# Kernel tuning notes

Measured on AMD Instinct MI355X. Metric: run time of the kernel, lower is better.

Reference implementation:

```python
import jax, jax.numpy as jnp
import numpy as np

NEG_SLOPE = 0.01
EPS = 1e-5


def _p(key, shape, scale=0.05):
    return jax.random.normal(key, shape, dtype=jnp.float32) * scale


def setup_inputs() -> dict:
    key = jax.random.key(0)
    ks = jax.random.split(key, 20)
    B, C0, N = 256, 160, 1024
    trees = jax.random.normal(ks[0], (B, C0, N), dtype=jnp.float32)
    indexes = jax.random.randint(ks[1], (B, 3 * N), 0, N)
    nodes = jax.random.randint(ks[2], (B,), 1, N + 1)
    dims = [(160, 256), (256, 128), (128, 64)]
    inp = {"trees": trees, "indexes": indexes, "nodes": nodes}
    for i, (ci, co) in enumerate(dims, start=1):
        inp[f"Wc{i}"] = _p(ks[2 + 4 * i], (co, ci, 3))   # tree-conv weight
        inp[f"bc{i}"] = jnp.zeros((co,), jnp.float32)
        inp[f"Wm{i}"] = _p(ks[3 + 4 * i], (co, ci))       # channel-mixer (1x1) weight
        inp[f"bm{i}"] = jnp.zeros((co,), jnp.float32)
    inp["W1"] = _p(ks[16], (64, 32))
    inp["b1"] = jnp.zeros((32,), jnp.float32)
    inp["W2"] = _p(ks[17], (32, 1))
    inp["b2"] = jnp.zeros((1,), jnp.float32)
    return inp


def _lero_block(x, idx, Wc, bc, Wm, bm):
    # x: [B, C, N], idx: [B, 3N] gather indices into node axis
    B, C, N = x.shape
    g = jnp.take_along_axis(x, idx[:, None, :], axis=2)          # [B, C, 3N]
    g = g.reshape(B, C, N, 3)                                    # parent/left/right triples
    y = jnp.einsum('bcnk,ock->bon', g, Wc) + bc[None, :, None]   # BinaryTreeConv
    mu = jnp.mean(y, axis=(1, 2), keepdims=True)                 # TreeLayerNorm (per-tree)
    sd = jnp.std(y, axis=(1, 2), keepdims=True, ddof=1)
    y = (y - mu) / (sd + EPS)
    xm = jnp.einsum('bcn,oc->bon', x, Wm) + bm[None, :, None]    # ChannelMixer
    return jax.nn.leaky_relu(xm + y, NEG_SLOPE)


def reference(trees, indexes, nodes,
              Wc1, bc1, Wm1, bm1,
              Wc2, bc2, Wm2, bm2,
              Wc3, bc3, Wm3, bm3,
              W1, b1, W2, b2):
    x = _lero_block(trees, indexes, Wc1, bc1, Wm1, bm1)
    x = _lero_block(x, indexes, Wc2, bc2, Wm2, bm2)
    x = _lero_block(x, indexes, Wc3, bc3, Wm3, bm3)   # [B, 64, N]
    N = x.shape[2]
    mask = jnp.arange(N)[None, :] < nodes[:, None]     # PreciseMaxPooling: mask padding
    pooled = jnp.max(jnp.where(mask[:, None, :], x, -jnp.inf), axis=2)  # [B, 64]
    h = jax.nn.leaky_relu(pooled @ W1 + b1, NEG_SLOPE)
    return h @ W2 + b2                                  # [B, 1]
```

## Files before the change

kernel.cpp:

```cpp
#include <hip/hip_runtime.h>
#include <stdint.h>

using f16 = _Float16;
typedef __attribute__((ext_vector_type(8))) f16 f16x8;
typedef __attribute__((ext_vector_type(4))) f16 f16x4;
typedef __attribute__((ext_vector_type(4))) float f32x4;

constexpr int N = 1024;

__device__ __forceinline__ float leaky(float v) { return v >= 0.f ? v : 0.01f * v; }

__device__ __forceinline__ void dma16(const void* g, void* l) {
    __builtin_amdgcn_global_load_lds(
        (const __attribute__((address_space(1))) uint32_t*)g,
        (__attribute__((address_space(3))) uint32_t*)l, 16, 0, 0);
}

template<int CI, int CO, int SEGS, int NSTG, int UW, int RT, bool ISMIX>
__global__ __launch_bounds__(512) void gemm_kernel(
    const f16* __restrict__ X, const int* __restrict__ idx,
    const f16* __restrict__ Wf, const float* __restrict__ bias,
    f16* __restrict__ Y, float2* __restrict__ part,
    const float2* __restrict__ pin, int nparts, float Mf)
{
    constexpr int SKT = SEGS * CI / 32;
    constexpr int KS32 = (SKT + NSTG - 1) / NSTG;
    constexpr int Ug = CO / 16;
    constexpr int NGRAN = KS32 * UW * 64;
    constexpr int SBYTES = NGRAN * 16;
    constexpr int EBYTES = 8 * 16 * 68 * 4;
    constexpr int LBYTES = SBYTES > EBYTES ? SBYTES : EBYTES;
    static_assert(CI % 32 == 0 && UW % 4 == 0, "geometry");
    static_assert(RT == 1 || RT == 2, "rt");

    __shared__ alignas(16) char ldsraw[LBYTES];
    __shared__ float redu[16];

    const int tid = threadIdx.x;
    const int w = tid >> 6, l = tid & 63;
    const int n0 = blockIdx.x * (128 * RT);
    const int u0 = blockIdx.y * UW;
    const int b  = blockIdx.z;
    const int g  = blockIdx.x + gridDim.x * blockIdx.y;

    int rows[RT][SEGS];
    #pragma unroll
    for (int rt = 0; rt < RT; ++rt) {
        int n = n0 + 16 * (RT * w + rt) + (l & 15);
        if constexpr (ISMIX) {
            rows[rt][0] = n;
        } else {
            const int* ip = idx + (size_t)b * 3 * N + 3 * n;
            #pragma unroll
            for (int s = 0; s < SEGS; ++s) rows[rt][s] = ip[s];
        }
    }
    const f16* xb = X + (size_t)b * N * CI;
    const int koff = 8 * (l >> 4);

    float2 st = make_float2(0.f, 0.f);
    if constexpr (ISMIX) {
        float s1 = 0.f, s2 = 0.f;
        for (int i = 0; i < nparts; ++i) {
            float2 p = pin[(size_t)b * 16 + i];
            s1 += p.x; s2 += p.y;
        }
        float mu = s1 / Mf;
        float var = fmaxf((s2 - s1 * s1 / Mf) / (Mf - 1.f), 0.f);
        st = make_float2(mu, 1.f / (sqrtf(var) + 1e-5f));
    }

    const f16* lds = (const f16*)ldsraw;

    auto stageW = [&](int pp) {
        for (int gg = tid; gg < NGRAN; gg += 512) {
            int skk = gg / (UW * 64);
            int uu = (gg >> 6) % UW;
            int ll = gg & 63;
            int skg = pp * KS32 + skk;
            if (skg < SKT)
                dma16(Wf + (((size_t)skg * Ug + u0 + uu) * 64 + ll) * 8,
                      ldsraw + (size_t)gg * 16);
        }
    };

    f16x8 pa[RT][3];
    auto loadA = [&](int sk, int d) {
        const int seg = (sk * 32) / CI;
        const int co = sk * 32 - seg * CI + koff;
        #pragma unroll
        for (int rt = 0; rt < RT; ++rt)
            pa[rt][d] = *(const f16x8*)(xb + (size_t)rows[rt][seg] * CI + co);
    };

    if constexpr (NSTG == 1) stageW(0);

    constexpr int D = SKT < 3 ? SKT : 3;
    #pragma unroll
    for (int d = 0; d < D; ++d) loadA(d, d);

    if constexpr (NSTG == 1) __syncthreads();

    f32x4 acc[RT][UW] = {};

    #pragma unroll
    for (int pp = 0; pp < NSTG; ++pp) {
        if constexpr (NSTG > 1) { stageW(pp); __syncthreads(); }

        #pragma unroll
        for (int skl = 0; skl < KS32; ++skl) {
            const int sk = pp * KS32 + skl;
            if (sk >= SKT) break;
            f16x8 av[RT];
            #pragma unroll
            for (int rt = 0; rt < RT; ++rt) av[rt] = pa[rt][sk % 3];
            if (sk + 3 < SKT) loadA(sk + 3, sk % 3);
            #pragma unroll
            for (int uu = 0; uu < UW; ++uu) {
                f16x8 wv = *(const f16x8*)(lds + ((size_t)(skl * UW + uu) * 64 + l) * 8);
                #pragma unroll
                for (int rt = 0; rt < RT; ++rt)
                    acc[rt][uu] = __builtin_amdgcn_mfma_f32_16x16x32_f16(av[rt], wv, acc[rt][uu], 0, 0, 0);
            }
        }
        if (pp + 1 < NSTG) __syncthreads();
    }

    __syncthreads();

    float (*ep)[68] = (float(*)[68])(ldsraw + w * 4352);
    float ps1 = 0.f, ps2 = 0.f;

    #pragma unroll
    for (int rt = 0; rt < RT; ++rt) {
        #pragma unroll
        for (int E = 0; E < UW / 4; ++E) {
            asm volatile("s_waitcnt lgkmcnt(0)" ::: "memory");
            #pragma unroll
            for (int u4 = 0; u4 < 4; ++u4)
                #pragma unroll
                for (int j = 0; j < 4; ++j)
                    ep[4 * (l >> 4) + j][u4 * 16 + (l & 15)] = acc[rt][E * 4 + u4][j];
            asm volatile("s_waitcnt lgkmcnt(0)" ::: "memory");
            __builtin_amdgcn_sched_barrier(0);
            #pragma unroll
            for (int ci = 0; ci < 2; ++ci) {
                int c = l + 64 * ci;
                int r = c >> 3, oc = (c & 7) * 8;
                int ob = u0 * 16 + E * 64 + oc;
                int n = n0 + 16 * (RT * w + rt) + r;
                size_t yoff = ((size_t)b * N + n) * CO + ob;
                float v[8];
                #pragma unroll
                for (int k = 0; k < 8; ++k) v[k] = ep[r][oc + k] + bias[ob + k];
                f16x8 rv;
                if constexpr (!ISMIX) {
                    #pragma unroll
                    for (int k = 0; k < 8; ++k) {
                        ps1 += v[k]; ps2 += v[k] * v[k];
                        rv[k] = (f16)v[k];
                    }
                } else {
                    f16x8 yc = *(const f16x8*)(Y + yoff);
                    #pragma unroll
                    for (int k = 0; k < 8; ++k)
                        rv[k] = (f16)leaky(v[k] + ((float)yc[k] - st.x) * st.y);
                }
                *(f16x8*)(Y + yoff) = rv;
            }
        }
    }

    if constexpr (!ISMIX) {
        #pragma unroll
        for (int m = 32; m; m >>= 1) { ps1 += __shfl_xor(ps1, m); ps2 += __shfl_xor(ps2, m); }
        if (l == 0) { redu[w * 2] = ps1; redu[w * 2 + 1] = ps2; }
        __syncthreads();
        if (tid == 0) {
            float t1 = 0.f, t2 = 0.f;
            #pragma unroll
            for (int k = 0; k < 8; ++k) { t1 += redu[2 * k]; t2 += redu[2 * k + 1]; }
            part[(size_t)b * 16 + g] = make_float2(t1, t2);
        }
    }
}

__global__ __launch_bounds__(256) void transpose_kernel(
    const float* __restrict__ trees, f16* __restrict__ X0)
{
    __shared__ f16 tile[32][68];
    int b = blockIdx.z, c0 = blockIdx.y * 32, n0 = blockIdx.x * 64;
    int tid = threadIdx.x;
    #pragma unroll
    for (int r = 0; r < 2; ++r) {
        int s = tid + 256 * r;
        int c = s >> 4, nq = (s & 15) * 4;
        float4 v = *(const float4*)&trees[((size_t)b * 160 + c0 + c) * N + n0 + nq];
        f16x4 h; h[0] = (f16)v.x; h[1] = (f16)v.y; h[2] = (f16)v.z; h[3] = (f16)v.w;
        *(f16x4*)&tile[c][nq] = h;
    }
    __syncthreads();
    int nn = tid >> 2, gc = tid & 3;
    f16x8 pack;
    #pragma unroll
    for (int e = 0; e < 8; ++e) pack[e] = tile[gc * 8 + e][nn];
    *(f16x8*)(X0 + ((size_t)b * N + n0 + nn) * 160 + c0 + gc * 8) = pack;
}

__device__ __forceinline__ void prepW_one(
    const float* __restrict__ Wsrc, f16* __restrict__ out,
    int e, int CO, int CI, int isconv)
{
    int j = e & 7, l = (e >> 3) & 63, r = e >> 9;
    int U = CO / 16;
    int u = r % U, t = r / U;
    int kap = 32 * t + 8 * (l >> 4) + j;
    int o = 16 * u + (l & 15);
    float v = isconv ? Wsrc[((size_t)o * CI + (kap % CI)) * 3 + kap / CI]
                     : Wsrc[(size_t)o * CI + kap];
    out[e] = (f16)v;
}

__global__ __launch_bounds__(256) void prepW6_kernel(
    const float* Wc1, const float* Wm1, const float* Wc2, const float* Wm2,
    const float* Wc3, const float* Wm3,
    f16* o1, f16* m1, f16* o2, f16* m2, f16* o3, f16* m3)
{
    int bx = blockIdx.x;
    if (bx < 480)       prepW_one(Wc1, o1, (bx -    0) * 256 + threadIdx.x, 256, 160, 1);
    else if (bx < 640)  prepW_one(Wm1, m1, (bx -  480) * 256 + threadIdx.x, 256, 160, 0);
    else if (bx < 1024) prepW_one(Wc2, o2, (bx -  640) * 256 + threadIdx.x, 128, 256, 1);
    else if (bx < 1152) prepW_one(Wm2, m2, (bx - 1024) * 256 + threadIdx.x, 128, 256, 0);
    else if (bx < 1248) prepW_one(Wc3, o3, (bx - 1152) * 256 + threadIdx.x,  64, 128, 1);
    else                prepW_one(Wm3, m3, (bx - 1248) * 256 + threadIdx.x,  64, 128, 0);
}

__global__ __launch_bounds__(256) void final_kernel(
    const f16* __restrict__ x3, const int* __restrict__ nodes,
    const float* __restrict__ W1, const float* __restrict__ b1,
    const float* __restrict__ W2, const float* __restrict__ b2,
    float* __restrict__ out)
{
    int b = blockIdx.x, tid = threadIdx.x;
    int oq = (tid & 7) * 8, rr = tid >> 3;
    int nv = nodes[b];
    const f16* p = x3 + (size_t)b * N * 64 + oq;
    float mx[8];
    #pragma unroll
    for (int k = 0; k < 8; ++k) mx[k] = -3.4e38f;
    for (int n = rr; n < nv; n += 32) {
        f16x8 v = *(const f16x8*)(p + (size_t)n * 64);
        #pragma unroll
        for (int k = 0; k < 8; ++k) mx[k] = fmaxf(mx[k], (float)v[k]);
    }
    __shared__ float pool[32][64];
    __shared__ float pooled[64], hbuf[32];
    #pragma unroll
    for (int k = 0; k < 8; ++k) pool[rr][oq + k] = mx[k];
    __syncthreads();
    if (tid < 64) {
        float m = pool[0][tid];
        #pragma unroll 8
        for (int r = 1; r < 32; ++r) m = fmaxf(m, pool[r][tid]);
        pooled[tid] = m;
    }
    __syncthreads();
    if (tid < 32) {
        float h = b1[tid];
        #pragma unroll 8
        for (int oo = 0; oo < 64; ++oo) h += pooled[oo] * W1[oo * 32 + tid];
        hbuf[tid] = leaky(h);
    }
    __syncthreads();
    if (tid == 0) {
        float rr2 = b2[0];
        for (int jj = 0; jj < 32; ++jj) rr2 += hbuf[jj] * W2[jj];
        out[b] = rr2;
    }
}

extern "C" void kernel_launch(void* const* d_in, const int* in_sizes, int n_in,
                              void* d_out, int out_size, void* d_ws, size_t ws_size,
                              hipStream_t stream)
{
    (void)in_sizes; (void)n_in; (void)out_size; (void)ws_size;
    const float* trees = (const float*)d_in[0];
    const int* indexes = (const int*)d_in[1];
    const int* nodes   = (const int*)d_in[2];
    const float* Wc1 = (const float*)d_in[3];
    const float* bc1 = (const float*)d_in[4];
    const float* Wm1 = (const float*)d_in[5];
    const float* bm1 = (const float*)d_in[6];
    const float* Wc2 = (const float*)d_in[7];
    const float* bc2 = (const float*)d_in[8];
    const float* Wm2 = (const float*)d_in[9];
    const float* bm2 = (const float*)d_in[10];
    const float* Wc3 = (const float*)d_in[11];
    const float* bc3 = (const float*)d_in[12];
    const float* Wm3 = (const float*)d_in[13];
    const float* bm3 = (const float*)d_in[14];
    const float* W1 = (const float*)d_in[15];
    const float* b1 = (const float*)d_in[16];
    const float* W2 = (const float*)d_in[17];
    const float* b2 = (const float*)d_in[18];
    float* out = (float*)d_out;

    char* ws = (char*)d_ws;
    f16* X0 = (f16*)ws;
    f16* A1 = (f16*)(ws + 83886080);
    f16* A2 = (f16*)ws;
    f16* A3 = A1;
    size_t toff = 218103808;
    f16* Wfc1 = (f16*)(ws + toff); toff += (size_t)480 * 256 * 2;
    f16* Wfm1 = (f16*)(ws + toff); toff += (size_t)160 * 256 * 2;
    f16* Wfc2 = (f16*)(ws + toff); toff += (size_t)768 * 128 * 2;
    f16* Wfm2 = (f16*)(ws + toff); toff += (size_t)256 * 128 * 2;
    f16* Wfc3 = (f16*)(ws + toff); toff += (size_t)384 * 64 * 2;
    f16* Wfm3 = (f16*)(ws + toff); toff += (size_t)128 * 64 * 2;
    float2* part  = (float2*)(ws + toff);

    transpose_kernel<<<dim3(16, 5, 256), 256, 0, stream>>>(trees, X0);
    prepW6_kernel<<<1280, 256, 0, stream>>>(Wc1, Wm1, Wc2, Wm2, Wc3, Wm3,
                                            Wfc1, Wfm1, Wfc2, Wfm2, Wfc3, Wfm3);

    gemm_kernel<160, 256, 3, 8, 16, 1, false><<<dim3(8, 1, 256), 512, 0, stream>>>(
        X0, indexes, Wfc1, bc1, A1, part, nullptr, 0, 0.f);
    gemm_kernel<160, 256, 1, 5, 16, 1, true><<<dim3(8, 1, 256), 512, 0, stream>>>(
        X0, nullptr, Wfm1, bm1, A1, nullptr, part, 8, 262144.f);

    gemm_kernel<256, 128, 3, 6, 8, 1, false><<<dim3(8, 1, 256), 512, 0, stream>>>(
        A1, indexes, Wfc2, bc2, A2, part, nullptr, 0, 0.f);
    gemm_kernel<256, 128, 1, 2, 8, 1, true><<<dim3(8, 1, 256), 512, 0, stream>>>(
        A1, nullptr, Wfm2, bm2, A2, nullptr, part, 8, 131072.f);

    gemm_kernel<128, 64, 3, 2, 4, 1, false><<<dim3(8, 1, 256), 512, 0, stream>>>(
        A2, indexes, Wfc3, bc3, A3, part, nullptr, 0, 0.f);
    gemm_kernel<128, 64, 1, 1, 4, 1, true><<<dim3(8, 1, 256), 512, 0, stream>>>(
        A2, nullptr, Wfm3, bm3, A3, nullptr, part, 8, 65536.f);

    final_kernel<<<256, 256, 0, stream>>>(A3, nodes, W1, b1, W2, b2, out);
}
```

Baseline: 415.5 us.

## Triple-buffer weight staging with vmcnt-based pipelining in tree-conv GEMMs

Adds a PIPE variant of the GEMM kernel that triple-buffers the weight tiles in LDS. It issues the weight DMA two stages ahead and the gathered-activation loads one stage ahead, then waits with explicit vmcnt counts instead of a full sync per stage. The three tree-conv launches use this path with more, smaller stages. This aims to overlap global and DMA latency with MFMA work, at the cost of more LDS, more activation registers and more barriers per block.

```diff
diff --git a/kernel.cpp b/kernel.cpp
--- a/kernel.cpp
+++ b/kernel.cpp
@@ -1,5 +1,6 @@
 #include <hip/hip_runtime.h>
 #include <stdint.h>
+#include <utility>
 
 using f16 = _Float16;
 typedef __attribute__((ext_vector_type(8))) f16 f16x8;
@@ -16,7 +17,26 @@
         (__attribute__((address_space(3))) uint32_t*)l, 16, 0, 0);
 }
 
-template<int CI, int CO, int SEGS, int NSTG, int UW, int RT, bool ISMIX>
+template<int A> __device__ __forceinline__ void wait_vm() {
+    asm volatile("s_waitcnt vmcnt(%0)" :: "n"(A) : "memory");
+}
+__device__ __forceinline__ void wait_lgkm0() {
+    asm volatile("s_waitcnt lgkmcnt(0)" ::: "memory");
+}
+
+template<int... Is, class F>
+__device__ __forceinline__ void static_for_impl(F&& f, std::integer_sequence<int, Is...>) {
+    (f(std::integral_constant<int, Is>{}), ...);
+}
+template<int Nn, class F>
+__device__ __forceinline__ void static_for(F&& f) {
+    static_for_impl(f, std::make_integer_sequence<int, Nn>{});
+}
+
+constexpr int cmin(int a, int b) { return a < b ? a : b; }
+constexpr int cmax(int a, int b) { return a > b ? a : b; }
+
+template<int CI, int CO, int SEGS, int NSTG, int UW, int RT, bool ISMIX, bool PIPE>
 __global__ __launch_bounds__(512) void gemm_kernel(
     const f16* __restrict__ X, const int* __restrict__ idx,
     const f16* __restrict__ Wf, const float* __restrict__ bias,
@@ -27,10 +47,13 @@
     constexpr int KS32 = (SKT + NSTG - 1) / NSTG;
     constexpr int Ug = CO / 16;
     constexpr int NGRAN = KS32 * UW * 64;
+    constexpr int SPW = NGRAN / 512;
     constexpr int SBYTES = NGRAN * 16;
+    constexpr int NBUF = PIPE ? 3 : 1;
     constexpr int EBYTES = 8 * 16 * 68 * 4;
-    constexpr int LBYTES = SBYTES > EBYTES ? SBYTES : EBYTES;
+    constexpr int LBYTES = (NBUF * SBYTES) > EBYTES ? (NBUF * SBYTES) : EBYTES;
     static_assert(CI % 32 == 0 && UW % 4 == 0, "geometry");
+    static_assert(!PIPE || (NSTG * KS32 == SKT && NGRAN % 512 == 0 && NSTG >= 3), "pipe");
     static_assert(RT == 1 || RT == 2, "rt");
 
     __shared__ alignas(16) char ldsraw[LBYTES];
@@ -70,66 +93,117 @@
         st = make_float2(mu, 1.f / (sqrtf(var) + 1e-5f));
     }
 
-    const f16* lds = (const f16*)ldsraw;
-
     auto stageW = [&](int pp) {
-        for (int gg = tid; gg < NGRAN; gg += 512) {
+        char* dst = ldsraw + (size_t)(pp % NBUF) * SBYTES;
+        #pragma unroll
+        for (int r = 0; r < SPW; ++r) {
+            int gg = tid + 512 * r;
             int skk = gg / (UW * 64);
             int uu = (gg >> 6) % UW;
             int ll = gg & 63;
             int skg = pp * KS32 + skk;
             if (skg < SKT)
                 dma16(Wf + (((size_t)skg * Ug + u0 + uu) * 64 + ll) * 8,
-                      ldsraw + (size_t)gg * 16);
+                      dst + (size_t)gg * 16);
         }
     };
 
-    f16x8 pa[RT][3];
-    auto loadA = [&](int sk, int d) {
-        const int seg = (sk * 32) / CI;
-        const int co = sk * 32 - seg * CI + koff;
-        #pragma unroll
-        for (int rt = 0; rt < RT; ++rt)
-            pa[rt][d] = *(const f16x8*)(xb + (size_t)rows[rt][seg] * CI + co);
-    };
-
-    if constexpr (NSTG == 1) stageW(0);
-
-    constexpr int D = SKT < 3 ? SKT : 3;
-    #pragma unroll
-    for (int d = 0; d < D; ++d) loadA(d, d);
-
-    if constexpr (NSTG == 1) __syncthreads();
-
     f32x4 acc[RT][UW] = {};
-
-    #pragma unroll
-    for (int pp = 0; pp < NSTG; ++pp) {
-        if constexpr (NSTG > 1) { stageW(pp); __syncthreads(); }
-
-        #pragma unroll
-        for (int skl = 0; skl < KS32; ++skl) {
-            const int sk = pp * KS32 + skl;
-            if (sk >= SKT) break;
-            f16x8 av[RT];
-            #pragma unroll
-            for (int rt = 0; rt < RT; ++rt) av[rt] = pa[rt][sk % 3];
-            if (sk + 3 < SKT) loadA(sk + 3, sk % 3);
-            #pragma unroll
-            for (int uu = 0; uu < UW; ++uu) {
-                f16x8 wv = *(const f16x8*)(lds + ((size_t)(skl * UW + uu) * 64 + l) * 8);
-                #pragma unroll
-                for (int rt = 0; rt < RT; ++rt)
-                    acc[rt][uu] = __builtin_amdgcn_mfma_f32_16x16x32_f16(av[rt], wv, acc[rt][uu], 0, 0, 0);
+    float ps1 = 0.f, ps2 = 0.f;
+
+    if constexpr (PIPE) {
+        constexpr int K = KS32;
+        constexpr int SLOTS = 2 * K;
+        f16x8 pa[RT][SLOTS];
+        auto loadA = [&](int sk, int slot) {
+            const int seg = (sk * 32) / CI;
+            const int co = sk * 32 - seg * CI + koff;
+            #pragma unroll
+            for (int rt = 0; rt < RT; ++rt)
+                pa[rt][slot] = *(const f16x8*)(xb + (size_t)rows[rt][seg] * CI + co);
+        };
+
+        stageW(0);
+        stageW(1);
+        static_for<K>([&](auto dc) {
+            constexpr int d = dc.value;
+            loadA(d, d % SLOTS);
+        });
+
+        static_for<NSTG>([&](auto tc) {
+            constexpr int t = tc.value;
+            if constexpr (t + 2 < NSTG) stageW(t + 2);
+            static_for<K>([&](auto ic) {
+                constexpr int j = (t + 1) * K + ic.value;
+                if constexpr (j < SKT) loadA(j, j % SLOTS);
+            });
+            constexpr int stagesAfter = cmin(2, NSTG - 1 - t);
+            constexpr int aGroups = cmax(0, cmin(t + 1, NSTG - 1) - cmax(t, 2) + 1);
+            constexpr int allow = SPW * stagesAfter + K * aGroups;
+            wait_vm<allow>();
+            __builtin_amdgcn_s_barrier();
+            __builtin_amdgcn_sched_barrier(0);
+            const f16* lw = (const f16*)(ldsraw + (size_t)(t % 3) * SBYTES);
+            static_for<K>([&](auto sc) {
+                constexpr int skl = sc.value;
+                constexpr int sk = t * K + skl;
+                f16x8 av[RT];
+                #pragma unroll
+                for (int rt = 0; rt < RT; ++rt) av[rt] = pa[rt][sk % SLOTS];
+                #pragma unroll
+                for (int uu = 0; uu < UW; ++uu) {
+                    f16x8 wv = *(const f16x8*)(lw + ((size_t)(skl * UW + uu) * 64 + l) * 8);
+                    #pragma unroll
+                    for (int rt = 0; rt < RT; ++rt)
+                        acc[rt][uu] = __builtin_amdgcn_mfma_f32_16x16x32_f16(av[rt], wv, acc[rt][uu], 0, 0, 0);
+                }
+            });
+            wait_lgkm0();
+            __builtin_amdgcn_s_barrier();
+        });
+    } else {
+        const f16* lds = (const f16*)ldsraw;
+        f16x8 pa[RT][3];
+        auto loadA = [&](int sk, int d) {
+            const int seg = (sk * 32) / CI;
+            const int co = sk * 32 - seg * CI + koff;
+            #pragma unroll
+            for (int rt = 0; rt < RT; ++rt)
+                pa[rt][d] = *(const f16x8*)(xb + (size_t)rows[rt][seg] * CI + co);
+        };
+
+        if constexpr (NSTG == 1) stageW(0);
+        constexpr int D = SKT < 3 ? SKT : 3;
+        #pragma unroll
+        for (int d = 0; d < D; ++d) loadA(d, d);
+        if constexpr (NSTG == 1) __syncthreads();
+
+        #pragma unroll
+        for (int pp = 0; pp < NSTG; ++pp) {
+            if constexpr (NSTG > 1) { stageW(pp); __syncthreads(); }
+            #pragma unroll
+            for (int skl = 0; skl < KS32; ++skl) {
+                const int sk = pp * KS32 + skl;
+                if (sk >= SKT) break;
+                f16x8 av[RT];
+                #pragma unroll
+                for (int rt = 0; rt < RT; ++rt) av[rt] = pa[rt][sk % 3];
+                if (sk + 3 < SKT) loadA(sk + 3, sk % 3);
+                #pragma unroll
+                for (int uu = 0; uu < UW; ++uu) {
+                    f16x8 wv = *(const f16x8*)(lds + ((size_t)(skl * UW + uu) * 64 + l) * 8);
+                    #pragma unroll
+                    for (int rt = 0; rt < RT; ++rt)
+                        acc[rt][uu] = __builtin_amdgcn_mfma_f32_16x16x32_f16(av[rt], wv, acc[rt][uu], 0, 0, 0);
+                }
             }
-        }
-        if (pp + 1 < NSTG) __syncthreads();
+            if (pp + 1 < NSTG) __syncthreads();
+        }
     }
 
     __syncthreads();
 
     float (*ep)[68] = (float(*)[68])(ldsraw + w * 4352);
-    float ps1 = 0.f, ps2 = 0.f;
 
     #pragma unroll
     for (int rt = 0; rt < RT; ++rt) {
@@ -323,19 +397,19 @@
     prepW6_kernel<<<1280, 256, 0, stream>>>(Wc1, Wm1, Wc2, Wm2, Wc3, Wm3,
                                             Wfc1, Wfm1, Wfc2, Wfm2, Wfc3, Wfm3);
 
-    gemm_kernel<160, 256, 3, 8, 16, 1, false><<<dim3(8, 1, 256), 512, 0, stream>>>(
+    gemm_kernel<160, 256, 3, 15, 16, 1, false, true><<<dim3(8, 1, 256), 512, 0, stream>>>(
         X0, indexes, Wfc1, bc1, A1, part, nullptr, 0, 0.f);
-    gemm_kernel<160, 256, 1, 5, 16, 1, true><<<dim3(8, 1, 256), 512, 0, stream>>>(
+    gemm_kernel<160, 256, 1, 5, 16, 1, true, false><<<dim3(8, 1, 256), 512, 0, stream>>>(
         X0, nullptr, Wfm1, bm1, A1, nullptr, part, 8, 262144.f);
 
-    gemm_kernel<256, 128, 3, 6, 8, 1, false><<<dim3(8, 1, 256), 512, 0, stream>>>(
+    gemm_kernel<256, 128, 3, 12, 8, 1, false, true><<<dim3(8, 1, 256), 512, 0, stream>>>(
         A1, indexes, Wfc2, bc2, A2, part, nullptr, 0, 0.f);
-    gemm_kernel<256, 128, 1, 2, 8, 1, true><<<dim3(8, 1, 256), 512, 0, stream>>>(
+    gemm_kernel<256, 128, 1, 2, 8, 1, true, false><<<dim3(8, 1, 256), 512, 0, stream>>>(
         A1, nullptr, Wfm2, bm2, A2, nullptr, part, 8, 131072.f);
 
-    gemm_kernel<128, 64, 3, 2, 4, 1, false><<<dim3(8, 1, 256), 512, 0, stream>>>(
+    gemm_kernel<128, 64, 3, 6, 4, 1, false, true><<<dim3(8, 1, 256), 512, 0, stream>>>(
         A2, indexes, Wfc3, bc3, A3, part, nullptr, 0, 0.f);
-    gemm_kernel<128, 64, 1, 1, 4, 1, true><<<dim3(8, 1, 256), 512, 0, stream>>>(
+    gemm_kernel<128, 64, 1, 1, 4, 1, true, false><<<dim3(8, 1, 256), 512, 0, stream>>>(
         A2, nullptr, Wfm3, bm3, A3, nullptr, part, 8, 65536.f);
 
     final_kernel<<<256, 256, 0, stream>>>(A3, nodes, W1, b1, W2, b2, out);
```

Measured after the change: 518.2 us. 1.25x slower.
